# Optimization experiments

Measured on AMD Instinct MI355X. Metric: run time of the kernel, lower is better.

## Reference

```python
import jax, jax.numpy as jnp
import numpy as np

D_MODEL = 2048
NUM_HEADS = 16
NUM_KV_HEADS = 4
HEAD_DIM = D_MODEL // NUM_HEADS  # 128
ROPE_THETA = 10000.0
BATCH = 2
SEQ = 2048


def _rotate_half(x):
    # interleaved rotate-half: pairs (x0,x1) -> (-x1, x0)
    x1 = x[..., ::2]
    x2 = x[..., 1::2]
    return jnp.stack((-x2, x1), axis=-1).reshape(x.shape)


def _rope_tables(seq_len, dtype, start_pos=0):
    inv_freq = 1.0 / (ROPE_THETA ** (jnp.arange(0, HEAD_DIM, 2, dtype=jnp.float32) / HEAD_DIM))
    positions = jnp.arange(start_pos, start_pos + seq_len, dtype=jnp.float32)
    freqs = jnp.outer(positions, inv_freq)              # [S, HD/2]
    emb = jnp.repeat(freqs, 2, axis=-1)                  # [S, HD]
    cos = jnp.cos(emb).astype(dtype)[None, None, :, :]   # [1,1,S,HD]
    sin = jnp.sin(emb).astype(dtype)[None, None, :, :]
    return cos, sin


def setup_inputs() -> dict:
    key = jax.random.key(0)
    ks = jax.random.split(key, 5)
    s = 0.02
    x = jax.random.normal(ks[0], (BATCH, SEQ, D_MODEL), dtype=jnp.float32)
    wq = jax.random.normal(ks[1], (D_MODEL, NUM_HEADS * HEAD_DIM), dtype=jnp.float32) * s
    wk = jax.random.normal(ks[2], (D_MODEL, NUM_KV_HEADS * HEAD_DIM), dtype=jnp.float32) * s
    wv = jax.random.normal(ks[3], (D_MODEL, NUM_KV_HEADS * HEAD_DIM), dtype=jnp.float32) * s
    wo = jax.random.normal(ks[4], (D_MODEL, D_MODEL), dtype=jnp.float32) * s
    return {"x": x, "wq": wq, "wk": wk, "wv": wv, "wo": wo}


def reference(x, wq, wk, wv, wo):
    batch, seq_len, _ = x.shape
    # projections (bias-free linears)
    q = (x @ wq).reshape(batch, seq_len, NUM_HEADS, HEAD_DIM).transpose(0, 2, 1, 3)
    k = (x @ wk).reshape(batch, seq_len, NUM_KV_HEADS, HEAD_DIM).transpose(0, 2, 1, 3)
    v = (x @ wv).reshape(batch, seq_len, NUM_KV_HEADS, HEAD_DIM).transpose(0, 2, 1, 3)
    # RoPE
    cos, sin = _rope_tables(seq_len, q.dtype)
    q = q * cos + _rotate_half(q) * sin
    k = k * cos + _rotate_half(k) * sin
    # GQA: duplicate KV heads
    repeats = NUM_HEADS // NUM_KV_HEADS
    k = jnp.repeat(k, repeats, axis=1)
    v = jnp.repeat(v, repeats, axis=1)
    # causal SDPA
    scale = HEAD_DIM ** -0.5
    scores = jnp.einsum('bhqd,bhkd->bhqk', q, k) * scale
    causal = jnp.tril(jnp.ones((seq_len, seq_len), dtype=bool))
    scores = jnp.where(causal[None, None, :, :], scores, -jnp.inf)
    weights = jax.nn.softmax(scores, axis=-1)
    y = jnp.einsum('bhqk,bhkd->bhqd', weights, v)
    y = y.transpose(0, 2, 1, 3).reshape(batch, seq_len, NUM_HEADS * HEAD_DIM)
    return y @ wo
```

## Files before the change

kernel.cpp:

```cpp
#include <hip/hip_runtime.h>
#include <cstdint>
#include <cstddef>

using short8 = __attribute__((ext_vector_type(8))) short;
using f32x4  = __attribute__((ext_vector_type(4))) float;
using u16x4  = __attribute__((ext_vector_type(4))) unsigned short;

#define DEV __device__ __forceinline__

DEV unsigned short f2bf(float f) {
  unsigned int u = __builtin_bit_cast(unsigned int, f);
  u += 0x7fffu + ((u >> 16) & 1u);
  return (unsigned short)(u >> 16);
}
DEV float bf2f(unsigned short h) {
  unsigned int u = ((unsigned int)h) << 16;
  return __builtin_bit_cast(float, u);
}
DEV unsigned int cvtpk_bf16(float lo, float hi) {
  unsigned int d;
  asm("v_cvt_pk_bf16_f32 %0, %1, %2" : "=v"(d) : "v"(lo), "v"(hi));
  return d;
}

#define GLL16(gp, lp)                                                          \
  __builtin_amdgcn_global_load_lds(                                            \
      (const __attribute__((address_space(1))) char*)(const char*)(gp),        \
      (__attribute__((address_space(3))) char*)(char*)(lp), 16, 0, 0)

constexpr int BATCH = 2, SEQ = 2048, DMODEL = 2048, NH = 16, NKVH = 4, DH = 128;
constexpr int MROWS = BATCH * SEQ;
constexpr int NQKV  = DMODEL + 2 * NKVH * DH;
constexpr int KOFF  = DMODEL;
constexpr int VOFF  = DMODEL + NKVH * DH;
constexpr float SM_L2 = 0.12751388158f;


__global__ void k_tables(float* __restrict__ tc, float* __restrict__ ts) {
  int id = blockIdx.x * 256 + threadIdx.x;
  int pos = id >> 6, i = id & 63;
  float freq = __expf(-(float)i * 0.14391157f);
  float ang = (float)pos * freq;
  tc[id] = cosf(ang);
  ts[id] = sinf(ang);
}

__global__ void k_castx(const float* __restrict__ x, unsigned short* __restrict__ xb) {
  int id = blockIdx.x * 256 + threadIdx.x;
  float4 v = ((const float4*)x)[id];
  u16x4 o = { f2bf(v.x), f2bf(v.y), f2bf(v.z), f2bf(v.w) };
  ((u16x4*)xb)[id] = o;
}

__global__ __launch_bounds__(256) void k_wtrans(const float* __restrict__ src,
                                                unsigned short* __restrict__ dst, int N) {
  __shared__ float tile[32][33];
  int n0 = blockIdx.x * 32, k0 = blockIdx.y * 32;
  int tx = threadIdx.x, ty = threadIdx.y;
  #pragma unroll
  for (int r = ty; r < 32; r += 8)
    tile[r][tx] = src[(size_t)(k0 + r) * N + n0 + tx];
  __syncthreads();
  #pragma unroll
  for (int r = ty; r < 32; r += 8)
    dst[(size_t)(n0 + r) * 2048 + k0 + tx] = f2bf(tile[tx][r]);
}

__global__ __launch_bounds__(256) void k_vtrans(const unsigned short* __restrict__ qkv,
                                                unsigned short* __restrict__ vt) {
  __shared__ unsigned short tile[32][33];
  int s0 = blockIdx.x * 32, d0 = blockIdx.y * 32;
  int bk = blockIdx.z;
  const unsigned short* src = qkv + (size_t)(bk >> 2) * SEQ * NQKV + VOFF + (bk & 3) * DH;
  unsigned short* dst = vt + ((size_t)bk * DH + d0) * SEQ + s0;
  int tx = threadIdx.x, ty = threadIdx.y;
  #pragma unroll
  for (int r = ty; r < 32; r += 8)
    tile[r][tx] = src[(size_t)(s0 + r) * NQKV + d0 + tx];
  __syncthreads();
  #pragma unroll
  for (int r = ty; r < 32; r += 8)
    dst[(size_t)r * SEQ + tx] = tile[tx][r];
}


template <int BNT, bool OUTF32, bool ROPE>
__global__ __launch_bounds__(512, 2) void k_gemm256(
    const unsigned short* __restrict__ A,
    const unsigned short* __restrict__ Bt,
    void* __restrict__ C, int M, int N, int K,
    const float* __restrict__ tc, const float* __restrict__ ts) {
  constexpr int NF = BNT / 64;
  constexpr int BLOADS = BNT / 64;
  __shared__ unsigned short As[2][256 * 64];
  __shared__ unsigned short Bs[2][BNT * 64];

  const int t = threadIdx.x, l = t & 63, w = t >> 6;
  const int rl = l & 15, kg = l >> 4;
  const int wm = w >> 2, wn = w & 3;

  const int gx = gridDim.x;
  const int nwg = gx * gridDim.y;
  const int idl = blockIdx.y * gx + blockIdx.x;
  const int swz = (idl & 7) * (nwg >> 3) + (idl >> 3);
  const int m0 = (swz / gx) * 256, n0 = (swz % gx) * BNT;

  const unsigned short* aSrc[4];
  const unsigned short* bSrc[BLOADS];
  #pragma unroll
  for (int i = 0; i < 4; ++i) {
    int c = i * 512 + t, row = c >> 3, q = c & 7;
    aSrc[i] = A + (size_t)(m0 + row) * K + ((q ^ (row & 7)) << 3);
  }
  #pragma unroll
  for (int i = 0; i < BLOADS; ++i) {
    int c = i * 512 + t, row = c >> 3, q = c & 7;
    bSrc[i] = Bt + (size_t)(n0 + row) * K + ((q ^ (row & 7)) << 3);
  }

  f32x4 acc[8][NF] = {};

  const int nk = K / 64;
  #pragma unroll
  for (int i = 0; i < 4; ++i) GLL16(aSrc[i], (char*)As[0] + i * 8192 + t * 16);
  #pragma unroll
  for (int i = 0; i < BLOADS; ++i) GLL16(bSrc[i], (char*)Bs[0] + i * 8192 + t * 16);

  int cur = 0;
  for (int kt = 0; kt < nk; ++kt) {
    if (kt + 1 < nk) {
      const int off = (kt + 1) * 64;
      #pragma unroll
      for (int i = 0; i < 4; ++i)
        GLL16(aSrc[i] + off, (char*)As[cur ^ 1] + i * 8192 + t * 16);
      #pragma unroll
      for (int i = 0; i < BLOADS; ++i)
        GLL16(bSrc[i] + off, (char*)Bs[cur ^ 1] + i * 8192 + t * 16);
      if constexpr (BNT == 256) asm volatile("s_waitcnt vmcnt(8)" ::: "memory");
      else                      asm volatile("s_waitcnt vmcnt(6)" ::: "memory");
    } else {
      asm volatile("s_waitcnt vmcnt(0)" ::: "memory");
    }
    __builtin_amdgcn_sched_barrier(0);
    __builtin_amdgcn_s_barrier();

    const unsigned short* a = As[cur];
    const unsigned short* b = Bs[cur];
    auto rdA = [&](int mf, int ks) {
      int row = wm * 128 + mf * 16 + rl;
      return *(const short8*)&a[row * 64 + (((ks * 4 + kg) ^ (row & 7)) << 3)];
    };
    auto rdB = [&](int nf, int ks) {
      int row = wn * (BNT / 4) + nf * 16 + rl;
      return *(const short8*)&b[row * 64 + (((ks * 4 + kg) ^ (row & 7)) << 3)];
    };

    short8 aF[4][2], bF[2][NF / 2][2];
    #pragma unroll
    for (int mi = 0; mi < 4; ++mi)
      #pragma unroll
      for (int ks = 0; ks < 2; ++ks) aF[mi][ks] = rdA(mi, ks);
    #pragma unroll
    for (int j = 0; j < NF / 2; ++j)
      #pragma unroll
      for (int ks = 0; ks < 2; ++ks) bF[0][j][ks] = rdB(j, ks);
    __builtin_amdgcn_s_setprio(1);
    #pragma unroll
    for (int mi = 0; mi < 4; ++mi)
      #pragma unroll
      for (int j = 0; j < NF / 2; ++j)
        #pragma unroll
        for (int ks = 0; ks < 2; ++ks)
          acc[mi][j] = __builtin_amdgcn_mfma_f32_16x16x32_bf16(aF[mi][ks], bF[0][j][ks], acc[mi][j], 0, 0, 0);
    __builtin_amdgcn_s_setprio(0);
    #pragma unroll
    for (int j = 0; j < NF / 2; ++j)
      #pragma unroll
      for (int ks = 0; ks < 2; ++ks) bF[1][j][ks] = rdB(NF / 2 + j, ks);
    __builtin_amdgcn_s_setprio(1);
    #pragma unroll
    for (int mi = 0; mi < 4; ++mi)
      #pragma unroll
      for (int j = 0; j < NF / 2; ++j)
        #pragma unroll
        for (int ks = 0; ks < 2; ++ks)
          acc[mi][NF / 2 + j] = __builtin_amdgcn_mfma_f32_16x16x32_bf16(aF[mi][ks], bF[1][j][ks], acc[mi][NF / 2 + j], 0, 0, 0);
    __builtin_amdgcn_s_setprio(0);
    #pragma unroll
    for (int mi = 0; mi < 4; ++mi)
      #pragma unroll
      for (int ks = 0; ks < 2; ++ks) aF[mi][ks] = rdA(4 + mi, ks);
    __builtin_amdgcn_s_setprio(1);
    #pragma unroll
    for (int mi = 0; mi < 4; ++mi)
      #pragma unroll
      for (int j = 0; j < NF / 2; ++j)
        #pragma unroll
        for (int ks = 0; ks < 2; ++ks)
          acc[4 + mi][j] = __builtin_amdgcn_mfma_f32_16x16x32_bf16(aF[mi][ks], bF[0][j][ks], acc[4 + mi][j], 0, 0, 0);
    __builtin_amdgcn_s_setprio(0);
    __builtin_amdgcn_s_setprio(1);
    #pragma unroll
    for (int mi = 0; mi < 4; ++mi)
      #pragma unroll
      for (int j = 0; j < NF / 2; ++j)
        #pragma unroll
        for (int ks = 0; ks < 2; ++ks)
          acc[4 + mi][NF / 2 + j] = __builtin_amdgcn_mfma_f32_16x16x32_bf16(aF[mi][ks], bF[1][j][ks], acc[4 + mi][NF / 2 + j], 0, 0, 0);
    __builtin_amdgcn_s_setprio(0);

    __builtin_amdgcn_s_barrier();
    cur ^= 1;
  }

  #pragma unroll
  for (int mf = 0; mf < 8; ++mf) {
    #pragma unroll
    for (int nf = 0; nf < NF; ++nf) {
      const int row0 = m0 + wm * 128 + mf * 16 + kg * 4;
      const int colb = n0 + wn * (BNT / 4) + nf * 16;
      const int col = colb + rl;
      if constexpr (ROPE) {
        if (colb < VOFF) {
          const int dd = (col & 127) >> 1;
          const float sgn = (col & 1) ? 1.0f : -1.0f;
          const float qs = (colb < KOFF) ? SM_L2 : 1.0f;
          #pragma unroll
          for (int r = 0; r < 4; ++r) {
            const int s = (row0 + r) & (SEQ - 1);
            const float c = tc[s * 64 + dd], sn = ts[s * 64 + dd];
            const float xv = acc[mf][nf][r];
            const float xp = __shfl_xor(xv, 1);
            acc[mf][nf][r] = (xv * c + sgn * xp * sn) * qs;
          }
        }
      }
      #pragma unroll
      for (int r = 0; r < 4; ++r) {
        if constexpr (OUTF32)
          ((float*)C)[(size_t)(row0 + r) * N + col] = acc[mf][nf][r];
        else
          ((unsigned short*)C)[(size_t)(row0 + r) * N + col] = f2bf(acc[mf][nf][r]);
      }
    }
  }
}


constexpr int QB = 128, KB = 64;
constexpr float THR = 8.0f;

__global__ __launch_bounds__(512, 4) void k_attn(const unsigned short* __restrict__ qkv,
                                                 const unsigned short* __restrict__ vt,
                                                 unsigned short* __restrict__ obuf) {
  __shared__ unsigned short Ks[2][KB * DH];
  __shared__ unsigned short Vs[2][DH * KB];
  __shared__ unsigned short Pw[8][16 * 64];

  const int t = threadIdx.x, l = t & 63, w = t >> 6;
  const int rl = l & 15, kg = l >> 4;

  const int id = blockIdx.x;
  const int b = id >> 8;
  const int u = id & 255;
  const int h = u >> 4;
  const int qtr = u & 15;
  const int qt = b ? (15 - qtr) : qtr;
  const int q0 = qt * QB;
  const int kvh = h >> 2;

  const unsigned short* qbase = qkv + (size_t)b * SEQ * NQKV;
  const unsigned short* kbase = qbase + KOFF + kvh * DH;
  const unsigned short* vtb = vt + (size_t)(b * NKVH + kvh) * DH * SEQ;

  const unsigned short* kp[2];
  const unsigned short* vp[2];
  #pragma unroll
  for (int i = 0; i < 2; ++i) {
    int c = i * 512 + t;
    int krow = c >> 4, kq = c & 15;
    kp[i] = kbase + (size_t)krow * NQKV + ((kq ^ (krow & 7)) << 3);
    int vrow = c >> 3, vq = c & 7;
    vp[i] = vtb + (size_t)vrow * SEQ + ((vq ^ (vrow & 7)) << 3);
  }

  const int qw0 = q0 + w * 16;

  short8 qF[4];
  {
    const size_t qr = (size_t)(qw0 + rl) * NQKV + h * DH;
    #pragma unroll
    for (int ks = 0; ks < 4; ++ks)
      qF[ks] = *(const short8*)(qbase + qr + ks * 32 + kg * 8);
  }

  f32x4 Oc[8] = {};
  float mr = -3e38f, lr = 0.f;

  char* pwB = (char*)Pw[w] + rl * 128;
  const int pkey = (rl & 7) << 4;
  const int nt = q0 / KB + 2;

  #pragma unroll
  for (int i = 0; i < 2; ++i) {
    GLL16(kp[i], (char*)Ks[0] + w * 1024 + i * 8192);
    GLL16(vp[i], (char*)Vs[0] + w * 1024 + i * 8192);
  }

  int cur = 0;
  for (int tt = 0; tt < nt; ++tt) {
    const int kv0 = tt * KB;
    const bool more = (tt + 1 < nt);
    if (more) {
      #pragma unroll
      for (int i = 0; i < 2; ++i) {
        GLL16(kp[i] + (size_t)(kv0 + KB) * NQKV, (char*)Ks[cur ^ 1] + w * 1024 + i * 8192);
        GLL16(vp[i] + (kv0 + KB),               (char*)Vs[cur ^ 1] + w * 1024 + i * 8192);
      }
      asm volatile("s_waitcnt vmcnt(4)" ::: "memory");
    } else {
      asm volatile("s_waitcnt vmcnt(0)" ::: "memory");
    }
    __builtin_amdgcn_sched_barrier(0);
    __builtin_amdgcn_s_barrier();

    if (kv0 < qw0 + 16) {
      const unsigned short* KsC = Ks[cur];
      const unsigned short* VsC = Vs[cur];

      f32x4 St[4] = {};
      __builtin_amdgcn_s_setprio(1);
      #pragma unroll
      for (int n = 0; n < 4; ++n) {
        const int kr = n * 16 + rl;
        #pragma unroll
        for (int ks = 0; ks < 4; ++ks) {
          short8 kF = *(const short8*)&KsC[kr * DH + (((ks * 4 + kg) ^ (kr & 7)) << 3)];
          St[n] = __builtin_amdgcn_mfma_f32_16x16x32_bf16(kF, qF[ks], St[n], 0, 0, 0);
        }
      }
      __builtin_amdgcn_s_setprio(0);

      float mx = -3e38f;
      const bool diag = (kv0 + KB - 1) > qw0;
      if (diag) {
        const int thr = qw0 + rl - kv0;
        #pragma unroll
        for (int n = 0; n < 4; ++n)
          #pragma unroll
          for (int r = 0; r < 4; ++r) {
            float s = St[n][r];
            if (n * 16 + kg * 4 + r > thr) s = -3e38f;
            St[n][r] = s;
            mx = fmaxf(mx, s);
          }
      } else {
        #pragma unroll
        for (int n = 0; n < 4; ++n)
          #pragma unroll
          for (int r = 0; r < 4; ++r) mx = fmaxf(mx, St[n][r]);
      }
      mx = fmaxf(mx, __shfl_xor(mx, 16));
      mx = fmaxf(mx, __shfl_xor(mx, 32));

      if (__any(mx > mr + THR)) {
        const float mnew = fmaxf(mr, mx);
        const float sf = exp2f(mr - mnew);
        mr = mnew;
        lr *= sf;
        float sfv[4];
        #pragma unroll
        for (int r = 0; r < 4; ++r) sfv[r] = __shfl(sf, kg * 4 + r, 16);
        #pragma unroll
        for (int c = 0; c < 8; ++c)
          #pragma unroll
          for (int r = 0; r < 4; ++r) Oc[c][r] *= sfv[r];
      }

      float rs = 0.f;
      #pragma unroll
      for (int n = 0; n < 4; ++n) {
        float e0 = exp2f(St[n][0] - mr);
        float e1 = exp2f(St[n][1] - mr);
        float e2 = exp2f(St[n][2] - mr);
        float e3 = exp2f(St[n][3] - mr);
        rs += (e0 + e1) + (e2 + e3);
        uint2 d;
        d.x = cvtpk_bf16(e0, e1);
        d.y = cvtpk_bf16(e2, e3);
        *(uint2*)(pwB + ((n * 32 + kg * 8) ^ pkey)) = d;
      }
      rs += __shfl_xor(rs, 16);
      rs += __shfl_xor(rs, 32);
      lr += rs;

      short8 pF[2];
      #pragma unroll
      for (int ks2 = 0; ks2 < 2; ++ks2)
        pF[ks2] = *(const short8*)(pwB + ((ks2 * 64 + kg * 16) ^ pkey));
      __builtin_amdgcn_s_setprio(1);
      #pragma unroll
      for (int c = 0; c < 8; ++c) {
        const int vr = c * 16 + rl;
        #pragma unroll
        for (int ks2 = 0; ks2 < 2; ++ks2) {
          short8 vF = *(const short8*)&VsC[vr * KB + (((ks2 * 4 + kg) ^ (vr & 7)) << 3)];
          Oc[c] = __builtin_amdgcn_mfma_f32_16x16x32_bf16(pF[ks2], vF, Oc[c], 0, 0, 0);
        }
      }
      __builtin_amdgcn_s_setprio(0);
    }

    __builtin_amdgcn_s_barrier();
    cur ^= 1;
  }

  const float linv = 1.0f / lr;
  float inv[4];
  #pragma unroll
  for (int r = 0; r < 4; ++r) inv[r] = __shfl(linv, kg * 4 + r, 16);
  #pragma unroll
  for (int c = 0; c < 8; ++c)
    #pragma unroll
    for (int r = 0; r < 4; ++r) {
      int row = b * SEQ + qw0 + kg * 4 + r;
      obuf[(size_t)row * DMODEL + h * DH + c * 16 + rl] = f2bf(Oc[c][r] * inv[r]);
    }
}


extern "C" void kernel_launch(void* const* d_in, const int* in_sizes, int n_in,
                              void* d_out, int out_size, void* d_ws, size_t ws_size,
                              hipStream_t stream) {
  const float* x  = (const float*)d_in[0];
  const float* wq = (const float*)d_in[1];
  const float* wk = (const float*)d_in[2];
  const float* wv = (const float*)d_in[3];
  const float* wo = (const float*)d_in[4];
  float* out = (float*)d_out;

  unsigned short* xb  = (unsigned short*)d_ws;
  unsigned short* wT  = xb  + (size_t)MROWS * DMODEL;
  unsigned short* woT = wT  + (size_t)NQKV * DMODEL;
  unsigned short* qkv = woT + (size_t)DMODEL * DMODEL;
  unsigned short* ob  = qkv + (size_t)MROWS * NQKV;
  float* tc = (float*)(ob + (size_t)MROWS * DMODEL);
  float* ts = tc + SEQ * 64;
  unsigned short* vtG = wT;

  k_tables<<<dim3(SEQ * 64 / 256), dim3(256), 0, stream>>>(tc, ts);
  k_castx<<<dim3(MROWS * DMODEL / 4 / 256), dim3(256), 0, stream>>>(x, xb);
  k_wtrans<<<dim3(DMODEL / 32, 64), dim3(32, 8), 0, stream>>>(wq, wT, DMODEL);
  k_wtrans<<<dim3(NKVH * DH / 32, 64), dim3(32, 8), 0, stream>>>(wk, wT + (size_t)DMODEL * 2048, NKVH * DH);
  k_wtrans<<<dim3(NKVH * DH / 32, 64), dim3(32, 8), 0, stream>>>(wv, wT + (size_t)VOFF * 2048, NKVH * DH);
  k_wtrans<<<dim3(DMODEL / 32, 64), dim3(32, 8), 0, stream>>>(wo, woT, DMODEL);

  k_gemm256<256, false, true><<<dim3(NQKV / 256, MROWS / 256), dim3(512), 0, stream>>>(
      xb, wT, qkv, MROWS, NQKV, DMODEL, tc, ts);
  k_vtrans<<<dim3(SEQ / 32, DH / 32, BATCH * NKVH), dim3(32, 8), 0, stream>>>(qkv, vtG);
  k_attn<<<dim3(512), dim3(512), 0, stream>>>(qkv, vtG, ob);
  k_gemm256<128, true, false><<<dim3(DMODEL / 128, MROWS / 256), dim3(512), 0, stream>>>(
      ob, woT, out, MROWS, DMODEL, DMODEL, nullptr, nullptr);
}
```

Before: 229.1 us.

## Process two 16-row query tiles per wave in attention with 4 waves per block

The attention block shrinks from 8 waves to 4, and each wave now handles 32 query rows as two 16-row MFMA tiles. Each K and V fragment read from shared memory is reused for two MFMAs, halving LDS traffic per unit of work. In exchange each wave holds roughly twice as many accumulator and score registers, fewer waves per block are available to hide latency, and causal skipping becomes coarser at 32-row granularity.

```diff
diff --git a/kernel.cpp b/kernel.cpp
--- a/kernel.cpp
+++ b/kernel.cpp
@@ -250,12 +250,12 @@
 constexpr int QB = 128, KB = 64;
 constexpr float THR = 8.0f;
 
-__global__ __launch_bounds__(512, 4) void k_attn(const unsigned short* __restrict__ qkv,
+__global__ __launch_bounds__(256, 2) void k_attn(const unsigned short* __restrict__ qkv,
                                                  const unsigned short* __restrict__ vt,
                                                  unsigned short* __restrict__ obuf) {
   __shared__ unsigned short Ks[2][KB * DH];
   __shared__ unsigned short Vs[2][DH * KB];
-  __shared__ unsigned short Pw[8][16 * 64];
+  __shared__ unsigned short Pw[4][32 * 64];
 
   const int t = threadIdx.x, l = t & 63, w = t >> 6;
   const int rl = l & 15, kg = l >> 4;
@@ -273,62 +273,63 @@
   const unsigned short* kbase = qbase + KOFF + kvh * DH;
   const unsigned short* vtb = vt + (size_t)(b * NKVH + kvh) * DH * SEQ;
 
-  const unsigned short* kp[2];
-  const unsigned short* vp[2];
-  #pragma unroll
-  for (int i = 0; i < 2; ++i) {
-    int c = i * 512 + t;
+  const unsigned short* kp[4];
+  const unsigned short* vp[4];
+  #pragma unroll
+  for (int i = 0; i < 4; ++i) {
+    int c = i * 256 + t;
     int krow = c >> 4, kq = c & 15;
     kp[i] = kbase + (size_t)krow * NQKV + ((kq ^ (krow & 7)) << 3);
     int vrow = c >> 3, vq = c & 7;
     vp[i] = vtb + (size_t)vrow * SEQ + ((vq ^ (vrow & 7)) << 3);
   }
 
-  const int qw0 = q0 + w * 16;
-
-  short8 qF[4];
-  {
-    const size_t qr = (size_t)(qw0 + rl) * NQKV + h * DH;
+  const int qw0 = q0 + w * 32;
+
+  short8 qF[2][4];
+  #pragma unroll
+  for (int m = 0; m < 2; ++m) {
+    const size_t qr = (size_t)(qw0 + m * 16 + rl) * NQKV + h * DH;
     #pragma unroll
     for (int ks = 0; ks < 4; ++ks)
-      qF[ks] = *(const short8*)(qbase + qr + ks * 32 + kg * 8);
-  }
-
-  f32x4 Oc[8] = {};
-  float mr = -3e38f, lr = 0.f;
-
-  char* pwB = (char*)Pw[w] + rl * 128;
+      qF[m][ks] = *(const short8*)(qbase + qr + ks * 32 + kg * 8);
+  }
+
+  f32x4 Oc[2][8] = {};
+  float mr[2] = { -3e38f, -3e38f }, lr[2] = { 0.f, 0.f };
+
+  char* pwB0 = (char*)Pw[w] + rl * 128;
+  char* pwB1 = pwB0 + 16 * 128;
   const int pkey = (rl & 7) << 4;
   const int nt = q0 / KB + 2;
 
   #pragma unroll
-  for (int i = 0; i < 2; ++i) {
-    GLL16(kp[i], (char*)Ks[0] + w * 1024 + i * 8192);
-    GLL16(vp[i], (char*)Vs[0] + w * 1024 + i * 8192);
+  for (int i = 0; i < 4; ++i) {
+    GLL16(kp[i], (char*)Ks[0] + i * 4096 + t * 16);
+    GLL16(vp[i], (char*)Vs[0] + i * 4096 + t * 16);
   }
 
   int cur = 0;
   for (int tt = 0; tt < nt; ++tt) {
     const int kv0 = tt * KB;
-    const bool more = (tt + 1 < nt);
-    if (more) {
-      #pragma unroll
-      for (int i = 0; i < 2; ++i) {
-        GLL16(kp[i] + (size_t)(kv0 + KB) * NQKV, (char*)Ks[cur ^ 1] + w * 1024 + i * 8192);
-        GLL16(vp[i] + (kv0 + KB),               (char*)Vs[cur ^ 1] + w * 1024 + i * 8192);
-      }
-      asm volatile("s_waitcnt vmcnt(4)" ::: "memory");
+    if (tt + 1 < nt) {
+      #pragma unroll
+      for (int i = 0; i < 4; ++i) {
+        GLL16(kp[i] + (size_t)(kv0 + KB) * NQKV, (char*)Ks[cur ^ 1] + i * 4096 + t * 16);
+        GLL16(vp[i] + (kv0 + KB),               (char*)Vs[cur ^ 1] + i * 4096 + t * 16);
+      }
+      asm volatile("s_waitcnt vmcnt(8)" ::: "memory");
     } else {
       asm volatile("s_waitcnt vmcnt(0)" ::: "memory");
     }
     __builtin_amdgcn_sched_barrier(0);
     __builtin_amdgcn_s_barrier();
 
-    if (kv0 < qw0 + 16) {
+    if (kv0 < qw0 + 32) {
       const unsigned short* KsC = Ks[cur];
       const unsigned short* VsC = Vs[cur];
 
-      f32x4 St[4] = {};
+      f32x4 St0[4] = {}, St1[4] = {};
       __builtin_amdgcn_s_setprio(1);
       #pragma unroll
       for (int n = 0; n < 4; ++n) {
@@ -336,68 +337,76 @@
         #pragma unroll
         for (int ks = 0; ks < 4; ++ks) {
           short8 kF = *(const short8*)&KsC[kr * DH + (((ks * 4 + kg) ^ (kr & 7)) << 3)];
-          St[n] = __builtin_amdgcn_mfma_f32_16x16x32_bf16(kF, qF[ks], St[n], 0, 0, 0);
+          St0[n] = __builtin_amdgcn_mfma_f32_16x16x32_bf16(kF, qF[0][ks], St0[n], 0, 0, 0);
+          St1[n] = __builtin_amdgcn_mfma_f32_16x16x32_bf16(kF, qF[1][ks], St1[n], 0, 0, 0);
         }
       }
       __builtin_amdgcn_s_setprio(0);
 
-      float mx = -3e38f;
-      const bool diag = (kv0 + KB - 1) > qw0;
-      if (diag) {
-        const int thr = qw0 + rl - kv0;
-        #pragma unroll
-        for (int n = 0; n < 4; ++n)
+      #pragma unroll
+      for (int m = 0; m < 2; ++m) {
+        f32x4* St = m ? St1 : St0;
+        char* pwB = m ? pwB1 : pwB0;
+        float mx = -3e38f;
+        const bool diag = (kv0 + KB - 1) > (qw0 + m * 16);
+        if (diag) {
+          const int thr = qw0 + m * 16 + rl - kv0;
           #pragma unroll
-          for (int r = 0; r < 4; ++r) {
-            float s = St[n][r];
-            if (n * 16 + kg * 4 + r > thr) s = -3e38f;
-            St[n][r] = s;
-            mx = fmaxf(mx, s);
-          }
-      } else {
-        #pragma unroll
-        for (int n = 0; n < 4; ++n)
+          for (int n = 0; n < 4; ++n)
+            #pragma unroll
+            for (int r = 0; r < 4; ++r) {
+              float s = St[n][r];
+              if (n * 16 + kg * 4 + r > thr) s = -3e38f;
+              St[n][r] = s;
+              mx = fmaxf(mx, s);
+            }
+        } else {
           #pragma unroll
-          for (int r = 0; r < 4; ++r) mx = fmaxf(mx, St[n][r]);
-      }
-      mx = fmaxf(mx, __shfl_xor(mx, 16));
-      mx = fmaxf(mx, __shfl_xor(mx, 32));
-
-      if (__any(mx > mr + THR)) {
-        const float mnew = fmaxf(mr, mx);
-        const float sf = exp2f(mr - mnew);
-        mr = mnew;
-        lr *= sf;
-        float sfv[4];
-        #pragma unroll
-        for (int r = 0; r < 4; ++r) sfv[r] = __shfl(sf, kg * 4 + r, 16);
-        #pragma unroll
-        for (int c = 0; c < 8; ++c)
+          for (int n = 0; n < 4; ++n)
+            #pragma unroll
+            for (int r = 0; r < 4; ++r) mx = fmaxf(mx, St[n][r]);
+        }
+        mx = fmaxf(mx, __shfl_xor(mx, 16));
+        mx = fmaxf(mx, __shfl_xor(mx, 32));
+
+        if (__any(mx > mr[m] + THR)) {
+          const float mnew = fmaxf(mr[m], mx);
+          const float sf = exp2f(mr[m] - mnew);
+          mr[m] = mnew;
+          lr[m] *= sf;
+          float sfv[4];
           #pragma unroll
-          for (int r = 0; r < 4; ++r) Oc[c][r] *= sfv[r];
-      }
-
-      float rs = 0.f;
-      #pragma unroll
-      for (int n = 0; n < 4; ++n) {
-        float e0 = exp2f(St[n][0] - mr);
-        float e1 = exp2f(St[n][1] - mr);
-        float e2 = exp2f(St[n][2] - mr);
-        float e3 = exp2f(St[n][3] - mr);
-        rs += (e0 + e1) + (e2 + e3);
-        uint2 d;
-        d.x = cvtpk_bf16(e0, e1);
-        d.y = cvtpk_bf16(e2, e3);
-        *(uint2*)(pwB + ((n * 32 + kg * 8) ^ pkey)) = d;
-      }
-      rs += __shfl_xor(rs, 16);
-      rs += __shfl_xor(rs, 32);
-      lr += rs;
-
-      short8 pF[2];
-      #pragma unroll
-      for (int ks2 = 0; ks2 < 2; ++ks2)
-        pF[ks2] = *(const short8*)(pwB + ((ks2 * 64 + kg * 16) ^ pkey));
+          for (int r = 0; r < 4; ++r) sfv[r] = __shfl(sf, kg * 4 + r, 16);
+          #pragma unroll
+          for (int c = 0; c < 8; ++c)
+            #pragma unroll
+            for (int r = 0; r < 4; ++r) Oc[m][c][r] *= sfv[r];
+        }
+
+        float rs = 0.f;
+        #pragma unroll
+        for (int n = 0; n < 4; ++n) {
+          float e0 = exp2f(St[n][0] - mr[m]);
+          float e1 = exp2f(St[n][1] - mr[m]);
+          float e2 = exp2f(St[n][2] - mr[m]);
+          float e3 = exp2f(St[n][3] - mr[m]);
+          rs += (e0 + e1) + (e2 + e3);
+          uint2 d;
+          d.x = cvtpk_bf16(e0, e1);
+          d.y = cvtpk_bf16(e2, e3);
+          *(uint2*)(pwB + ((n * 32 + kg * 8) ^ pkey)) = d;
+        }
+        rs += __shfl_xor(rs, 16);
+        rs += __shfl_xor(rs, 32);
+        lr[m] += rs;
+      }
+
+      short8 pF0[2], pF1[2];
+      #pragma unroll
+      for (int ks2 = 0; ks2 < 2; ++ks2) {
+        pF0[ks2] = *(const short8*)(pwB0 + ((ks2 * 64 + kg * 16) ^ pkey));
+        pF1[ks2] = *(const short8*)(pwB1 + ((ks2 * 64 + kg * 16) ^ pkey));
+      }
       __builtin_amdgcn_s_setprio(1);
       #pragma unroll
       for (int c = 0; c < 8; ++c) {
@@ -405,7 +414,8 @@
         #pragma unroll
         for (int ks2 = 0; ks2 < 2; ++ks2) {
           short8 vF = *(const short8*)&VsC[vr * KB + (((ks2 * 4 + kg) ^ (vr & 7)) << 3)];
-          Oc[c] = __builtin_amdgcn_mfma_f32_16x16x32_bf16(pF[ks2], vF, Oc[c], 0, 0, 0);
+          Oc[0][c] = __builtin_amdgcn_mfma_f32_16x16x32_bf16(pF0[ks2], vF, Oc[0][c], 0, 0, 0);
+          Oc[1][c] = __builtin_amdgcn_mfma_f32_16x16x32_bf16(pF1[ks2], vF, Oc[1][c], 0, 0, 0);
         }
       }
       __builtin_amdgcn_s_setprio(0);
@@ -415,17 +425,20 @@
     cur ^= 1;
   }
 
-  const float linv = 1.0f / lr;
-  float inv[4];
-  #pragma unroll
-  for (int r = 0; r < 4; ++r) inv[r] = __shfl(linv, kg * 4 + r, 16);
-  #pragma unroll
-  for (int c = 0; c < 8; ++c)
-    #pragma unroll
-    for (int r = 0; r < 4; ++r) {
-      int row = b * SEQ + qw0 + kg * 4 + r;
-      obuf[(size_t)row * DMODEL + h * DH + c * 16 + rl] = f2bf(Oc[c][r] * inv[r]);
-    }
+  #pragma unroll
+  for (int m = 0; m < 2; ++m) {
+    const float linv = 1.0f / lr[m];
+    float inv[4];
+    #pragma unroll
+    for (int r = 0; r < 4; ++r) inv[r] = __shfl(linv, kg * 4 + r, 16);
+    #pragma unroll
+    for (int c = 0; c < 8; ++c)
+      #pragma unroll
+      for (int r = 0; r < 4; ++r) {
+        int row = b * SEQ + qw0 + m * 16 + kg * 4 + r;
+        obuf[(size_t)row * DMODEL + h * DH + c * 16 + rl] = f2bf(Oc[m][c][r] * inv[r]);
+      }
+  }
 }
 
 
@@ -458,7 +471,7 @@
   k_gemm256<256, false, true><<<dim3(NQKV / 256, MROWS / 256), dim3(512), 0, stream>>>(
       xb, wT, qkv, MROWS, NQKV, DMODEL, tc, ts);
   k_vtrans<<<dim3(SEQ / 32, DH / 32, BATCH * NKVH), dim3(32, 8), 0, stream>>>(qkv, vtG);
-  k_attn<<<dim3(512), dim3(512), 0, stream>>>(qkv, vtG, ob);
+  k_attn<<<dim3(512), dim3(256), 0, stream>>>(qkv, vtG, ob);
   k_gemm256<128, true, false><<<dim3(DMODEL / 128, MROWS / 256), dim3(512), 0, stream>>>(
       ob, woT, out, MROWS, DMODEL, DMODEL, nullptr, nullptr);
 }
```

Result: slower. 237.9 us (+3.9%).
